# Kernel tuning notes

Hardware: AMD Instinct MI355X
Metric: run time of the kernel (lower is better)

Reference implementation:

```python
import jax, jax.numpy as jnp
import numpy as np
from jax import lax

B, L, D = 2, 4096, 2048
H = 16
DK = D // H  # head qk dim == head v dim == 128
CONV = 4
EPS = 1e-5


def _causal_depthwise_conv(x, w):
    # x: [b, l, c], w: [c, K]; torch-style cross-correlation with left padding K-1
    K = w.shape[1]
    xp = jnp.pad(x, ((0, 0), (K - 1, 0), (0, 0)))
    Lx = x.shape[1]
    y = jnp.zeros_like(x)
    for i in range(K):
        y = y + xp[:, i:i + Lx, :] * w[:, i]
    return y


def _l2norm(x):
    return x / jnp.sqrt(jnp.sum(x * x, axis=-1, keepdims=True) + 1e-12)


def _delta_rule(q, k, v, beta):
    # q,k: [b,h,l,dk]; v: [b,h,l,dv]; beta: [b,h,l]
    b, h, l, dk = q.shape
    dv = v.shape[-1]
    qs = jnp.moveaxis(q, 2, 0)
    ks = jnp.moveaxis(k, 2, 0)
    vs = jnp.moveaxis(v, 2, 0)
    bs = jnp.moveaxis(beta, 2, 0)

    def step(S, inp):
        qt, kt, vt, bt = inp  # [b,h,dk],[b,h,dk],[b,h,dv],[b,h]
        kS = jnp.einsum('bhk,bhkv->bhv', kt, S)
        u = bt[..., None] * (vt - kS)
        S = S + kt[..., None] * u[:, :, None, :]
        o = jnp.einsum('bhk,bhkv->bhv', qt, S)
        return S, o

    S0 = jnp.zeros((b, h, dk, dv), dtype=q.dtype)
    _, os = lax.scan(step, S0, (qs, ks, vs, bs))
    return jnp.moveaxis(os, 0, 2)  # [b,h,l,dv]


def setup_inputs() -> dict:
    key = jax.random.key(0)
    ks = jax.random.split(key, 8)
    s = 0.02
    return {
        'hidden_states': jax.random.normal(ks[0], (B, L, D), jnp.float32),
        'w_cattn': jax.random.normal(ks[1], (D, 3 * D), jnp.float32) * s,
        'wq_conv': jax.random.normal(ks[2], (D, CONV), jnp.float32) * 0.3,
        'wk_conv': jax.random.normal(ks[3], (D, CONV), jnp.float32) * 0.3,
        'wv_conv': jax.random.normal(ks[4], (D, CONV), jnp.float32) * 0.3,
        'w_beta': jax.random.normal(ks[5], (D, H), jnp.float32) * s,
        'o_norm_w': jnp.ones((DK,), jnp.float32),
        'w_o': jax.random.normal(ks[6], (D, D), jnp.float32) * s,
    }


def reference(hidden_states, w_cattn, wq_conv, wk_conv, wv_conv, w_beta, o_norm_w, w_o):
    qkv = hidden_states @ w_cattn  # [b,l,3D]
    q, k, v = jnp.split(qkv, 3, axis=-1)
    # short conv + SiLU activation (qk_activation='silu', v conv always SiLU)
    q = jax.nn.silu(_causal_depthwise_conv(q, wq_conv))
    k = jax.nn.silu(_causal_depthwise_conv(k, wk_conv))
    v = jax.nn.silu(_causal_depthwise_conv(v, wv_conv))
    # b l (h d) -> b h l d
    def to_heads(x):
        return jnp.transpose(x.reshape(B, L, H, -1), (0, 2, 1, 3))
    q, k, v = to_heads(q), to_heads(k), to_heads(v)
    # qk_norm = 'l2'
    q = _l2norm(q)
    k = _l2norm(k)
    beta = jax.nn.sigmoid(hidden_states @ w_beta)  # [b,l,h]
    beta = jnp.transpose(beta, (0, 2, 1))  # [b,h,l]
    o = _delta_rule(q, k, v, beta)  # [b,h,l,dv]
    o = jnp.transpose(o, (0, 2, 1, 3))  # [b,l,h,dv]
    # RMSNorm over head_v_dim
    o = o * lax.rsqrt(jnp.mean(o * o, axis=-1, keepdims=True) + EPS) * o_norm_w
    o = o.reshape(B, L, D)
    return o @ w_o
```

## Files before the change

### kernel.cpp

```cpp
#include <hip/hip_runtime.h>
#include <stdint.h>

#define B_   2
#define L_   4096
#define D_   2048
#define H_   16
#define DK_  128
#define ND3  6144
#define BL_  8192

typedef __bf16 bf16x8 __attribute__((ext_vector_type(8)));
typedef float  f32x4  __attribute__((ext_vector_type(4)));

__device__ __forceinline__ float bf2f(ushort u){ return __uint_as_float(((unsigned)u)<<16); }
__device__ __forceinline__ ushort f2bf(float f){
  unsigned u = __float_as_uint(f);
  unsigned r = u + 0x7FFFu + ((u>>16)&1u);
  return (ushort)(r>>16);
}
__device__ __forceinline__ f32x4 mfma16(bf16x8 a, bf16x8 b, f32x4 c){
  return __builtin_amdgcn_mfma_f32_16x16x32_bf16(a, b, c, 0, 0, 0);
}

#define BAR_LGKM() do{ __builtin_amdgcn_sched_barrier(0); \
  asm volatile("s_waitcnt lgkmcnt(0)" ::: "memory"); \
  __builtin_amdgcn_s_barrier(); \
  __builtin_amdgcn_sched_barrier(0);}while(0)
#define BAR_VMALL() do{ __builtin_amdgcn_sched_barrier(0); \
  asm volatile("s_waitcnt vmcnt(0) lgkmcnt(0)" ::: "memory"); \
  __builtin_amdgcn_s_barrier(); \
  __builtin_amdgcn_sched_barrier(0);}while(0)

__global__ __launch_bounds__(256) void k_cast(const float* __restrict__ x, ushort* __restrict__ y, int n4){
  int i = blockIdx.x*blockDim.x + threadIdx.x;
  int stride = gridDim.x*blockDim.x;
  for (; i < n4; i += stride){
    float4 v = ((const float4*)x)[i];
    ushort4 o; o.x=f2bf(v.x); o.y=f2bf(v.y); o.z=f2bf(v.z); o.w=f2bf(v.w);
    ((ushort4*)y)[i] = o;
  }
}

__global__ __launch_bounds__(256) void k_transpose_cast(const float* __restrict__ in, ushort* __restrict__ out,
                                                        int R, int C){
  __shared__ float tile[32][33];
  int c0 = blockIdx.x*32, r0 = blockIdx.y*32;
  int tx = threadIdx.x, ty = threadIdx.y;
  #pragma unroll
  for (int i=0;i<32;i+=8) tile[ty+i][tx] = in[(size_t)(r0+ty+i)*C + (c0+tx)];
  __syncthreads();
  #pragma unroll
  for (int i=0;i<32;i+=8) out[(size_t)(c0+ty+i)*R + (r0+tx)] = f2bf(tile[tx][ty+i]);
}

template<int OUT_BF16>
__global__ __launch_bounds__(512, 1) void k_gemmks(const ushort* __restrict__ A, const ushort* __restrict__ Bt,
                                                   void* __restrict__ Cv, int M, int N, int K){
  __shared__ ushort LDSB[65536];
  char* lds = (char*)LDSB;
  const int tid = threadIdx.x, lane = tid & 63, w = tid >> 6;
  const int wm = w >> 2, wn = w & 3;
  int nwg = gridDim.x*gridDim.y;
  int id  = blockIdx.y*gridDim.x + blockIdx.x;
  int sw  = ((nwg & 7) == 0) ? ((id & 7)*(nwg >> 3) + (id >> 3)) : id;
  const int bx = sw % gridDim.x, by = sw / gridDim.x;
  const int m0 = by*256, n0 = bx*256;
  const int NT = K >> 6;
  const int NP = NT*2;
  const size_t rowb = (size_t)K*2;

  f32x4 acc[8][4];
  #pragma unroll
  for (int i=0;i<8;i++)
    #pragma unroll
    for (int j=0;j<4;j++) acc[i][j] = (f32x4){0.f,0.f,0.f,0.f};

  const int c0 = tid, c1 = tid + 512;
  const int r0c = ((c0>>6)<<4) + (c0&15), h0 = (c0>>4)&3;
  const int r1c = ((c1>>6)<<4) + (c1&15), h1 = (c1>>4)&3;
  const char* gA = (const char*)A  + (size_t)m0*rowb;
  const char* gB = (const char*)Bt + (size_t)n0*rowb;

  auto stage = [&](int slot, int tile, int s){
    const char* ga = gA + (size_t)tile*128 + s*64;
    const char* gb = gB + (size_t)tile*128 + s*64;
    char* la = lds + slot*32768;
    char* lb = la + 16384;
    __builtin_amdgcn_global_load_lds((const __attribute__((address_space(1))) void*)(ga + (size_t)r0c*rowb + h0*16),
                                     (__attribute__((address_space(3))) void*)(la + c0*16), 16, 0, 0);
    __builtin_amdgcn_global_load_lds((const __attribute__((address_space(1))) void*)(ga + (size_t)r1c*rowb + h1*16),
                                     (__attribute__((address_space(3))) void*)(la + c1*16), 16, 0, 0);
    __builtin_amdgcn_global_load_lds((const __attribute__((address_space(1))) void*)(gb + (size_t)r0c*rowb + h0*16),
                                     (__attribute__((address_space(3))) void*)(lb + c0*16), 16, 0, 0);
    __builtin_amdgcn_global_load_lds((const __attribute__((address_space(1))) void*)(gb + (size_t)r1c*rowb + h1*16),
                                     (__attribute__((address_space(3))) void*)(lb + c1*16), 16, 0, 0);
  };

  stage(0, 0, 0);
  stage(1, 0, 1);
  stage(2, 1, 0);
  __builtin_amdgcn_sched_barrier(0);
  asm volatile("s_waitcnt vmcnt(8)" ::: "memory");
  __builtin_amdgcn_s_barrier();
  __builtin_amdgcn_sched_barrier(0);

  for (int pb = 0; pb < NP; pb += 4){
    #pragma unroll
    for (int q = 0; q < 4; ++q){
      const int p = pb + q;
      const char* base = lds + q*32768;
      bf16x8 af[8], bfr[4];
      #pragma unroll
      for (int i=0;i<4;i++) af[i]  = *(const bf16x8*)(base + (wm*128 + i*16)*64 + lane*16);
      #pragma unroll
      for (int j=0;j<4;j++) bfr[j] = *(const bf16x8*)(base + 16384 + (wn*64 + j*16)*64 + lane*16);
      __builtin_amdgcn_sched_barrier(0);
      #pragma unroll
      for (int i=4;i<8;i++) af[i]  = *(const bf16x8*)(base + (wm*128 + i*16)*64 + lane*16);
      {
        int ps = p + 3;
        int tile = ps >> 1; if (tile >= NT) tile = NT - 1;
        stage(ps & 3, tile, ps & 1);
      }
      __builtin_amdgcn_sched_barrier(0);
      asm volatile("s_waitcnt lgkmcnt(4)" ::: "memory");
      __builtin_amdgcn_sched_barrier(0);
      __builtin_amdgcn_s_setprio(1);
      #pragma unroll
      for (int i=0;i<4;i++)
        #pragma unroll
        for (int j=0;j<4;j++)
          acc[i][j] = mfma16(af[i], bfr[j], acc[i][j]);
      __builtin_amdgcn_sched_barrier(0);
      asm volatile("s_waitcnt lgkmcnt(0)" ::: "memory");
      __builtin_amdgcn_sched_barrier(0);
      #pragma unroll
      for (int i=4;i<8;i++)
        #pragma unroll
        for (int j=0;j<4;j++)
          acc[i][j] = mfma16(af[i], bfr[j], acc[i][j]);
      __builtin_amdgcn_s_setprio(0);
      __builtin_amdgcn_sched_barrier(0);
      asm volatile("s_waitcnt vmcnt(8)" ::: "memory");
      __builtin_amdgcn_s_barrier();
      __builtin_amdgcn_sched_barrier(0);
    }
  }

  const int rbase = m0 + wm*128 + (lane>>4)*4;
  const int cbase = n0 + wn*64 + (lane&15);
  #pragma unroll
  for (int fi=0;fi<8;fi++)
    #pragma unroll
    for (int fj=0;fj<4;fj++)
      #pragma unroll
      for (int r=0;r<4;r++){
        int row = rbase + fi*16 + r;
        int col = cbase + fj*16;
        float v = acc[fi][fj][r];
        if (OUT_BF16) ((ushort*)Cv)[(size_t)row*N + col] = f2bf(v);
        else          ((float*) Cv)[(size_t)row*N + col] = v;
      }
}

__global__ __launch_bounds__(256) void k_wbt(const float* __restrict__ wb, ushort* __restrict__ wbT){
  int d = blockIdx.x*256 + threadIdx.x;
  #pragma unroll
  for (int h=0;h<16;h++) wbT[(size_t)h*2048 + d] = f2bf(wb[(size_t)d*16 + h]);
}

__global__ __launch_bounds__(64) void k_beta2(const ushort* __restrict__ A16, const ushort* __restrict__ wbT,
                                              float* __restrict__ beta){
  const int rt = blockIdx.x;
  const int lane = threadIdx.x;
  const int lr = lane & 15, lk8 = (lane>>4)*8;
  const int r0 = rt*16;
  f32x4 acc0 = (f32x4){0.f,0.f,0.f,0.f};
  f32x4 acc1 = (f32x4){0.f,0.f,0.f,0.f};
  for (int k0=0; k0<2048; k0+=64){
    bf16x8 a0 = *(const bf16x8*)&A16[(size_t)(r0+lr)*2048 + k0 + lk8];
    bf16x8 b0 = *(const bf16x8*)&wbT[(size_t)lr*2048 + k0 + lk8];
    bf16x8 a1 = *(const bf16x8*)&A16[(size_t)(r0+lr)*2048 + k0 + 32 + lk8];
    bf16x8 b1 = *(const bf16x8*)&wbT[(size_t)lr*2048 + k0 + 32 + lk8];
    acc0 = mfma16(a0, b0, acc0);
    acc1 = mfma16(a1, b1, acc1);
  }
  const int h = lane & 15;
  const int rbase = r0 + (lane>>4)*4;
  #pragma unroll
  for (int r=0;r<4;r++){
    int row = rbase + r;
    int b = row >> 12, l = row & 4095;
    float sg = 1.f/(1.f + __expf(-(acc0[r] + acc1[r])));
    beta[((size_t)(b*H_ + h))*L_ + l] = sg;
  }
}

__global__ __launch_bounds__(256) void k_conv2(const ushort* __restrict__ qkv,
      const float* __restrict__ wq, const float* __restrict__ wk, const float* __restrict__ wv,
      ushort* __restrict__ QH, ushort* __restrict__ KH, ushort* __restrict__ VH){
  const int seg = blockIdx.x, part = blockIdx.y, b = blockIdx.z;
  const int t = threadIdx.x;
  const int ch = t*8;
  const int h = t >> 4, d0 = (t & 15)*8;
  const float* wc = (part==0) ? wq : (part==1) ? wk : wv;
  ushort* outs = ((part==0) ? QH : (part==1) ? KH : VH)
                 + ((size_t)(b*H_ + h)*L_)*DK_ + d0;
  const ushort* inp = qkv + ((size_t)b*L_)*ND3 + part*D_ + ch;

  float wgt[4][8];
  #pragma unroll
  for (int j=0;j<8;j++){
    float4 w4 = *(const float4*)&wc[(ch + j)*4];
    wgt[0][j]=w4.x; wgt[1][j]=w4.y; wgt[2][j]=w4.z; wgt[3][j]=w4.w;
  }

  const int l0 = seg*32;
  float x0[8], x1[8], x2[8];
  {
    float* dsts[3] = {x0, x1, x2};
    #pragma unroll
    for (int i=0;i<3;i++){
      int l = l0 - 3 + i;
      float* d = dsts[i];
      if (l >= 0){
        const ushort* p = inp + (size_t)l*ND3;
        ushort4 a = *(const ushort4*)p, c = *(const ushort4*)(p+4);
        d[0]=bf2f(a.x); d[1]=bf2f(a.y); d[2]=bf2f(a.z); d[3]=bf2f(a.w);
        d[4]=bf2f(c.x); d[5]=bf2f(c.y); d[6]=bf2f(c.z); d[7]=bf2f(c.w);
      } else {
        #pragma unroll
        for (int j=0;j<8;j++) d[j] = 0.f;
      }
    }
  }

  for (int i=0;i<32;i++){
    const int l = l0 + i;
    float cur[8];
    {
      const ushort* p = inp + (size_t)l*ND3;
      ushort4 a = *(const ushort4*)p, c = *(const ushort4*)(p+4);
      cur[0]=bf2f(a.x); cur[1]=bf2f(a.y); cur[2]=bf2f(a.z); cur[3]=bf2f(a.w);
      cur[4]=bf2f(c.x); cur[5]=bf2f(c.y); cur[6]=bf2f(c.z); cur[7]=bf2f(c.w);
    }
    float y[8]; float ss = 0.f;
    #pragma unroll
    for (int j=0;j<8;j++){
      float yy = x0[j]*wgt[0][j] + x1[j]*wgt[1][j] + x2[j]*wgt[2][j] + cur[j]*wgt[3][j];
      yy = yy / (1.f + __expf(-yy));
      y[j] = yy; ss += yy*yy;
    }
    if (part < 2){
      #pragma unroll
      for (int m=1;m<16;m<<=1) ss += __shfl_xor(ss, m, 64);
      float sc = rsqrtf(ss + 1e-12f);
      #pragma unroll
      for (int j=0;j<8;j++) y[j] *= sc;
    }
    ushort4 o0, o1;
    o0.x=f2bf(y[0]); o0.y=f2bf(y[1]); o0.z=f2bf(y[2]); o0.w=f2bf(y[3]);
    o1.x=f2bf(y[4]); o1.y=f2bf(y[5]); o1.z=f2bf(y[6]); o1.w=f2bf(y[7]);
    ushort* op = outs + (size_t)l*DK_;
    *(ushort4*)op = o0; *(ushort4*)(op+4) = o1;
    #pragma unroll
    for (int j=0;j<8;j++){ x0[j]=x1[j]; x1[j]=x2[j]; x2[j]=cur[j]; }
  }
}

__global__ __launch_bounds__(64) void k_prep(const ushort* __restrict__ QH, const ushort* __restrict__ KH,
      const float* __restrict__ BETA, ushort* __restrict__ TB, ushort* __restrict__ MM,
      ushort* __restrict__ KT){
  const int bid = blockIdx.x, bh = bid>>6, c = bid&63;
  const int lane = threadIdx.x;
  __shared__ ushort Ks[64][136];
  __shared__ __align__(16) char QA[17408];
  __shared__ float bs[64];
  ushort (*Qs)[136] = (ushort (*)[136])QA;
  float  (*As)[64]  = (float  (*)[64])QA;

  const ushort* kg = KH + ((size_t)bh*L_ + c*64)*DK_;
  const ushort* qg = QH + ((size_t)bh*L_ + c*64)*DK_;
  {
    const uint4* ks4 = (const uint4*)(kg + (size_t)lane*DK_);
    const uint4* qs4 = (const uint4*)(qg + (size_t)lane*DK_);
    uint4* kd = (uint4*)&Ks[lane][0];
    uint4* qd = (uint4*)&Qs[lane][0];
    #pragma unroll
    for (int i=0;i<16;i++){ kd[i] = ks4[i]; qd[i] = qs4[i]; }
    bs[lane] = BETA[(size_t)bh*L_ + c*64 + lane];
  }
  __syncthreads();
  const int lr = lane&15, lk = lane>>4;

  f32x4 gac[4][4];
  #pragma unroll
  for (int i=0;i<4;i++)
    #pragma unroll
    for (int j=0;j<4;j++) gac[i][j] = (f32x4){0.f,0.f,0.f,0.f};
  #pragma unroll
  for (int kk=0;kk<4;kk++){
    bf16x8 fr[4];
    #pragma unroll
    for (int i=0;i<4;i++) fr[i] = *(const bf16x8*)&Ks[i*16+lr][kk*32 + lk*8];
    #pragma unroll
    for (int mi=0;mi<4;mi++)
      #pragma unroll
      for (int ni=0;ni<4;ni++)
        gac[mi][ni] = mfma16(fr[mi], fr[ni], gac[mi][ni]);
  }
  {
    f32x4 mac[4][4];
    #pragma unroll
    for (int i=0;i<4;i++)
      #pragma unroll
      for (int j=0;j<4;j++) mac[i][j] = (f32x4){0.f,0.f,0.f,0.f};
    #pragma unroll
    for (int kk=0;kk<4;kk++){
      bf16x8 frq[4], frk[4];
      #pragma unroll
      for (int i=0;i<4;i++){
        frq[i] = *(const bf16x8*)&Qs[i*16+lr][kk*32 + lk*8];
        frk[i] = *(const bf16x8*)&Ks[i*16+lr][kk*32 + lk*8];
      }
      #pragma unroll
      for (int mi=0;mi<4;mi++)
        #pragma unroll
        for (int ni=0;ni<4;ni++)
          mac[mi][ni] = mfma16(frq[mi], frk[ni], mac[mi][ni]);
    }
    #pragma unroll
    for (int mi=0;mi<4;mi++)
      #pragma unroll
      for (int ni=0;ni<4;ni++)
        #pragma unroll
        for (int r=0;r<4;r++){
          int t = mi*16 + lk*4 + r, s = ni*16 + lr;
          float v = (s <= t) ? mac[mi][ni][r] : 0.f;
          MM[(size_t)bid*4096 + t*64 + s] = f2bf(v);
        }
  }
  __syncthreads();

  #pragma unroll
  for (int mi=0;mi<4;mi++)
    #pragma unroll
    for (int ni=0;ni<4;ni++)
      #pragma unroll
      for (int r=0;r<4;r++){
        int t = mi*16 + lk*4 + r, s = ni*16 + lr;
        As[t][s] = (s < t) ? (bs[t] * gac[mi][ni][r]) : 0.f;
      }
  __syncthreads();

  float rT[64];
  #pragma unroll
  for (int t=0;t<64;t++){
    float arow = As[t][lane];
    float a = (t==lane) ? 1.f : 0.f;
    #pragma unroll
    for (int s=0;s<t;s++){
      float cc = __int_as_float(__builtin_amdgcn_readlane(__float_as_int(arow), s));
      a -= cc * rT[s];
    }
    rT[t] = a;
  }
  {
    float bc = bs[lane];
    #pragma unroll
    for (int t=0;t<64;t++)
      TB[(size_t)bid*4096 + t*64 + lane] = f2bf(rT[t] * bc);
  }
  for (int d2=0; d2<64; d2++){
    unsigned uu = *(const unsigned*)&Ks[lane][2*d2];
    KT[(size_t)bid*8192 + (size_t)(2*d2)*64 + lane]   = (ushort)(uu & 0xffffu);
    KT[(size_t)bid*8192 + (size_t)(2*d2+1)*64 + lane] = (ushort)(uu >> 16);
  }
}

template<int LRB, int GRB, int NB, int XM>
__device__ __forceinline__ void stage_swz(const ushort* __restrict__ g, ushort* l,
                                          int colOff, int w, int lane){
  for (int idx = w; idx < NB/1024; idx += 4){
    int off = idx*1024 + lane*16;
    int row = off / LRB;
    int inner = off & (LRB-1);
    int src = row*GRB + colOff + (inner ^ ((row&XM)<<4));
    __builtin_amdgcn_global_load_lds(
      (const __attribute__((address_space(1))) void*)((const char*)g + src),
      (__attribute__((address_space(3))) void*)((char*)l + idx*1024), 16, 0, 0);
  }
}

__global__ __launch_bounds__(256) void k_chunkrec(const ushort* __restrict__ QH, const ushort* __restrict__ KH,
      const ushort* __restrict__ VH, const ushort* __restrict__ TB, const ushort* __restrict__ MM,
      const ushort* __restrict__ KT, ushort* __restrict__ OH){
  const int p = blockIdx.x;
  const int xg = p & 7, slot = p >> 3;
  const int bh = xg + (slot >> 2)*8;
  const int vq = slot & 3;
  const int tid = threadIdx.x, lane = tid&63, w = tid>>6;
  const int lr = lane&15, lk = lane>>4;
  const int tw = w*16;
  const int dw = w*32;

  __shared__ ushort SM[77824];
  ushort* Stl = SM + 69632;
  ushort* Ztl = SM + 73728;
  ushort* Utl = SM + 75776;

  const ushort* kbase  = KH + ((size_t)bh*L_)*DK_;
  const ushort* qbase  = QH + ((size_t)bh*L_)*DK_;
  const ushort* vbase  = VH + ((size_t)bh*L_)*DK_;
  const ushort* tbase  = TB + ((size_t)bh*64)*4096;
  const ushort* mbase  = MM + ((size_t)bh*64)*4096;
  const ushort* ktbase = KT + ((size_t)bh*64)*8192;
  ushort* obase = OH + ((size_t)bh*L_)*DK_ + vq*32;

  auto stageall = [&](ushort* buf, int c){
    stage_swz<256,256,16384,7>(kbase  + (size_t)c*8192, buf,         0,     w, lane);
    stage_swz<256,256,16384,7>(qbase  + (size_t)c*8192, buf + 8192,  0,     w, lane);
    stage_swz<128,128,16384,7>(ktbase + (size_t)c*8192, buf + 16384, 0,     w, lane);
    stage_swz<128,128, 8192,7>(tbase  + (size_t)c*4096, buf + 24576, 0,     w, lane);
    stage_swz<128,128, 8192,7>(mbase  + (size_t)c*4096, buf + 28672, 0,     w, lane);
    stage_swz< 64,256, 4096,3>(vbase  + (size_t)c*8192, buf + 32768, vq*64, w, lane);
  };

  f32x4 Stf[2][2];
  #pragma unroll
  for (int a=0;a<2;a++)
    #pragma unroll
    for (int b=0;b<2;b++) Stf[a][b] = (f32x4){0.f,0.f,0.f,0.f};

  stageall(SM, 0);
  BAR_VMALL();

  for (int c=0; c<64; ++c){
    ushort* buf  = SM + (c&1)*34816;
    ushort* nbuf = SM + ((c+1)&1)*34816;
    const ushort* Kc  = buf;
    const ushort* Qc  = buf + 8192;
    const ushort* Ktc = buf + 16384;
    const ushort* Tbc = buf + 24576;
    const ushort* Mc  = buf + 28672;
    const ushort* Vc  = buf + 32768;

    if (c+1 < 64) stageall(nbuf, c+1);

    #pragma unroll
    for (int mj=0;mj<2;mj++)
      #pragma unroll
      for (int nd=0;nd<2;nd++)
        #pragma unroll
        for (int r=0;r<4;r++){
          int j = mj*16 + lk*4 + r;
          int d = dw + nd*16 + lr;
          Stl[j*128 + (d ^ ((j&7)<<3))] = f2bf(Stf[mj][nd][r]);
        }
    BAR_LGKM();

    f32x4 xac[2];
    xac[0] = (f32x4){0.f,0.f,0.f,0.f}; xac[1] = (f32x4){0.f,0.f,0.f,0.f};
    #pragma unroll
    for (int kk=0;kk<4;kk++){
      int e = kk*32 + lk*8;
      int ta = tw + lr;
      bf16x8 ak = *(const bf16x8*)&Kc[ta*128 + (e ^ ((ta&7)<<3))];
      #pragma unroll
      for (int ni=0;ni<2;ni++){
        int j = ni*16 + lr;
        bf16x8 bst = *(const bf16x8*)&Stl[j*128 + (e ^ ((j&7)<<3))];
        xac[ni] = mfma16(ak, bst, xac[ni]);
      }
    }
    #pragma unroll
    for (int ni=0;ni<2;ni++)
      #pragma unroll
      for (int r=0;r<4;r++){
        int t = tw + lk*4 + r;
        int j = ni*16 + lr;
        float v = bf2f(Vc[t*32 + (j ^ ((t&3)<<3))]);
        Ztl[j*64 + (t ^ ((j&7)<<3))] = f2bf(v - xac[ni][r]);
      }
    BAR_LGKM();

    f32x4 uac[2];
    uac[0] = (f32x4){0.f,0.f,0.f,0.f}; uac[1] = (f32x4){0.f,0.f,0.f,0.f};
    #pragma unroll
    for (int kk=0;kk<2;kk++){
      int e = kk*32 + lk*8;
      int ta = tw + lr;
      bf16x8 at = *(const bf16x8*)&Tbc[ta*64 + (e ^ ((ta&7)<<3))];
      #pragma unroll
      for (int ni=0;ni<2;ni++){
        int j = ni*16 + lr;
        bf16x8 bz = *(const bf16x8*)&Ztl[j*64 + (e ^ ((j&7)<<3))];
        uac[ni] = mfma16(at, bz, uac[ni]);
      }
    }
    #pragma unroll
    for (int ni=0;ni<2;ni++)
      #pragma unroll
      for (int r=0;r<4;r++){
        int t = tw + lk*4 + r;
        int j = ni*16 + lr;
        Utl[j*64 + (t ^ ((j&7)<<3))] = f2bf(uac[ni][r]);
      }
    BAR_LGKM();

    f32x4 oac[2];
    oac[0] = (f32x4){0.f,0.f,0.f,0.f}; oac[1] = (f32x4){0.f,0.f,0.f,0.f};
    #pragma unroll
    for (int kk=0;kk<4;kk++){
      int e = kk*32 + lk*8;
      int ta = tw + lr;
      bf16x8 aq = *(const bf16x8*)&Qc[ta*128 + (e ^ ((ta&7)<<3))];
      #pragma unroll
      for (int ni=0;ni<2;ni++){
        int j = ni*16 + lr;
        bf16x8 bst = *(const bf16x8*)&Stl[j*128 + (e ^ ((j&7)<<3))];
        oac[ni] = mfma16(aq, bst, oac[ni]);
      }
    }
    #pragma unroll
    for (int kk=0;kk<2;kk++){
      int e = kk*32 + lk*8;
      int ta = tw + lr;
      bf16x8 am = *(const bf16x8*)&Mc[ta*64 + (e ^ ((ta&7)<<3))];
      #pragma unroll
      for (int ni=0;ni<2;ni++){
        int j = ni*16 + lr;
        bf16x8 bu = *(const bf16x8*)&Utl[j*64 + (e ^ ((j&7)<<3))];
        oac[ni] = mfma16(am, bu, oac[ni]);
      }
    }
    #pragma unroll
    for (int ni=0;ni<2;ni++)
      #pragma unroll
      for (int r=0;r<4;r++){
        int t = tw + lk*4 + r;
        int j = ni*16 + lr;
        obase[(size_t)(c*64 + t)*DK_ + j] = f2bf(oac[ni][r]);
      }

    #pragma unroll
    for (int kk=0;kk<2;kk++){
      int e = kk*32 + lk*8;
      bf16x8 au[2], bk[2];
      #pragma unroll
      for (int mj=0;mj<2;mj++){ int j = mj*16 + lr; au[mj] = *(const bf16x8*)&Utl[j*64 + (e ^ ((j&7)<<3))]; }
      #pragma unroll
      for (int nd=0;nd<2;nd++){ int d = dw + nd*16 + lr; bk[nd] = *(const bf16x8*)&Ktc[d*64 + (e ^ ((d&7)<<3))]; }
      #pragma unroll
      for (int mj=0;mj<2;mj++)
        #pragma unroll
        for (int nd=0;nd<2;nd++)
          Stf[mj][nd] = mfma16(au[mj], bk[nd], Stf[mj][nd]);
    }
    BAR_VMALL();
  }
}

__global__ __launch_bounds__(256) void k_norm(const ushort* __restrict__ OH, const float* __restrict__ gw,
                                              ushort* __restrict__ O2){
  const int blk = blockIdx.x;
  const int b = blk >> 12, l = blk & 4095;
  const int t = threadIdx.x;
  const int h = t >> 4, d0 = (t & 15) * 8;
  const ushort* ip = OH + ((size_t)(b*H_ + h)*L_ + l)*DK_ + d0;
  ushort4 a = *(const ushort4*)ip, c = *(const ushort4*)(ip+4);
  float x[8];
  x[0]=bf2f(a.x); x[1]=bf2f(a.y); x[2]=bf2f(a.z); x[3]=bf2f(a.w);
  x[4]=bf2f(c.x); x[5]=bf2f(c.y); x[6]=bf2f(c.z); x[7]=bf2f(c.w);
  float ss = 0.f;
  #pragma unroll
  for (int j=0;j<8;j++) ss += x[j]*x[j];
  #pragma unroll
  for (int m=1;m<16;m<<=1) ss += __shfl_xor(ss, m, 64);
  float sc = rsqrtf(ss * (1.f/128.f) + 1e-5f);
  ushort* opp = O2 + (size_t)blk*D_ + h*DK_ + d0;
  ushort4 o0, o1;
  o0.x=f2bf(x[0]*sc*gw[d0+0]); o0.y=f2bf(x[1]*sc*gw[d0+1]);
  o0.z=f2bf(x[2]*sc*gw[d0+2]); o0.w=f2bf(x[3]*sc*gw[d0+3]);
  o1.x=f2bf(x[4]*sc*gw[d0+4]); o1.y=f2bf(x[5]*sc*gw[d0+5]);
  o1.z=f2bf(x[6]*sc*gw[d0+6]); o1.w=f2bf(x[7]*sc*gw[d0+7]);
  *(ushort4*)opp = o0; *(ushort4*)(opp+4) = o1;
}

extern "C" void kernel_launch(void* const* d_in, const int* in_sizes, int n_in,
                              void* d_out, int out_size, void* d_ws, size_t ws_size,
                              hipStream_t stream) {
  (void)in_sizes; (void)n_in; (void)out_size; (void)ws_size;
  const float* hidden  = (const float*)d_in[0];
  const float* w_cattn = (const float*)d_in[1];
  const float* wq_conv = (const float*)d_in[2];
  const float* wk_conv = (const float*)d_in[3];
  const float* wv_conv = (const float*)d_in[4];
  const float* w_beta  = (const float*)d_in[5];
  const float* o_nw    = (const float*)d_in[6];
  const float* w_o     = (const float*)d_in[7];
  float* out = (float*)d_out;

  char* W = (char*)d_ws;
  ushort* A16   = (ushort*)(W);
  ushort* WcatT = (ushort*)(W + 33554432u);
  ushort* WoT   = (ushort*)(W + 33554432u);
  float*  BETA  = (float*) (W + 41943040u);
  ushort* WBT   = (ushort*)(W + 42467328u);
  ushort* QKV   = (ushort*)(W + 58720256u);
  ushort* TB    = (ushort*)(W + 58720256u);
  ushort* MM    = (ushort*)(W + 75497472u);
  ushort* KT    = (ushort*)(W + 92274688u);
  ushort* O2    = (ushort*)(W + 125829120u);
  ushort* QH    = (ushort*)(W + 159383552u);
  ushort* KH    = (ushort*)(W + 192937984u);
  ushort* VH    = (ushort*)(W + 226492416u);
  ushort* OH = A16;

  k_cast<<<4096, 256, 0, stream>>>(hidden, A16, (BL_*D_)/4);
  k_transpose_cast<<<dim3(ND3/32, D_/32), dim3(32,8), 0, stream>>>(w_cattn, WcatT, D_, ND3);
  k_gemmks<1><<<dim3(ND3/256, BL_/256), 512, 0, stream>>>(A16, WcatT, QKV, BL_, ND3, D_);
  k_transpose_cast<<<dim3(D_/32, D_/32), dim3(32,8), 0, stream>>>(w_o, WoT, D_, D_);
  k_wbt<<<8, 256, 0, stream>>>(w_beta, WBT);
  k_beta2<<<512, 64, 0, stream>>>(A16, WBT, BETA);
  k_conv2<<<dim3(128, 3, 2), 256, 0, stream>>>(QKV, wq_conv, wk_conv, wv_conv, QH, KH, VH);
  k_prep<<<2048, 64, 0, stream>>>(QH, KH, BETA, TB, MM, KT);
  k_chunkrec<<<128, 256, 0, stream>>>(QH, KH, VH, TB, MM, KT, OH);
  k_norm<<<BL_, 256, 0, stream>>>(OH, o_nw, O2);
  k_gemmks<0><<<dim3(D_/256, BL_/256), 512, 0, stream>>>(O2, WoT, out, BL_, D_, D_);
}
```

Baseline: 614.3 us.

## Split chunk recurrence across 8 value slices per head to double block count

The chunked delta-rule recurrence kernel now splits each head's value dimension into 8 slices of 16 columns instead of 4 slices of 32. This doubles the grid from 128 to 256 blocks so more compute units on the GPU are busy, and it halves per-block MFMA work and shared memory. In exchange, each block still loads the full K, Q, K-transpose, T and M chunk tiles, so redundant global-to-LDS traffic for those shared operands doubles.

```diff
diff --git a/kernel.cpp b/kernel.cpp
--- a/kernel.cpp
+++ b/kernel.cpp
@@ -396,18 +396,18 @@
       const ushort* __restrict__ VH, const ushort* __restrict__ TB, const ushort* __restrict__ MM,
       const ushort* __restrict__ KT, ushort* __restrict__ OH){
   const int p = blockIdx.x;
-  const int xg = p & 7, slot = p >> 3;
-  const int bh = xg + (slot >> 2)*8;
-  const int vq = slot & 3;
+  const int xg = p & 7, s = p >> 3;
+  const int bh = xg + (s >> 3)*8;
+  const int vo = s & 7;
   const int tid = threadIdx.x, lane = tid&63, w = tid>>6;
   const int lr = lane&15, lk = lane>>4;
   const int tw = w*16;
   const int dw = w*32;
 
-  __shared__ ushort SM[77824];
-  ushort* Stl = SM + 69632;
-  ushort* Ztl = SM + 73728;
-  ushort* Utl = SM + 75776;
+  __shared__ ushort SM[71680];
+  ushort* Stl = SM + 67584;
+  ushort* Ztl = SM + 69632;
+  ushort* Utl = SM + 70656;
 
   const ushort* kbase  = KH + ((size_t)bh*L_)*DK_;
   const ushort* qbase  = QH + ((size_t)bh*L_)*DK_;
@@ -415,7 +415,7 @@
   const ushort* tbase  = TB + ((size_t)bh*64)*4096;
   const ushort* mbase  = MM + ((size_t)bh*64)*4096;
   const ushort* ktbase = KT + ((size_t)bh*64)*8192;
-  ushort* obase = OH + ((size_t)bh*L_)*DK_ + vq*32;
+  ushort* obase = OH + ((size_t)bh*L_)*DK_ + vo*16;
 
   auto stageall = [&](ushort* buf, int c){
     stage_swz<256,256,16384,7>(kbase  + (size_t)c*8192, buf,         0,     w, lane);
@@ -423,21 +423,19 @@
     stage_swz<128,128,16384,7>(ktbase + (size_t)c*8192, buf + 16384, 0,     w, lane);
     stage_swz<128,128, 8192,7>(tbase  + (size_t)c*4096, buf + 24576, 0,     w, lane);
     stage_swz<128,128, 8192,7>(mbase  + (size_t)c*4096, buf + 28672, 0,     w, lane);
-    stage_swz< 64,256, 4096,3>(vbase  + (size_t)c*8192, buf + 32768, vq*64, w, lane);
+    stage_swz< 32,256, 2048,0>(vbase  + (size_t)c*8192, buf + 32768, vo*32, w, lane);
   };
 
-  f32x4 Stf[2][2];
-  #pragma unroll
-  for (int a=0;a<2;a++)
-    #pragma unroll
-    for (int b=0;b<2;b++) Stf[a][b] = (f32x4){0.f,0.f,0.f,0.f};
+  f32x4 Stf[2];
+  Stf[0] = (f32x4){0.f,0.f,0.f,0.f};
+  Stf[1] = (f32x4){0.f,0.f,0.f,0.f};
 
   stageall(SM, 0);
   BAR_VMALL();
 
   for (int c=0; c<64; ++c){
-    ushort* buf  = SM + (c&1)*34816;
-    ushort* nbuf = SM + ((c+1)&1)*34816;
+    ushort* buf  = SM + (c&1)*33792;
+    ushort* nbuf = SM + ((c+1)&1)*33792;
     const ushort* Kc  = buf;
     const ushort* Qc  = buf + 8192;
     const ushort* Ktc = buf + 16384;
@@ -448,114 +446,84 @@
     if (c+1 < 64) stageall(nbuf, c+1);
 
     #pragma unroll
-    for (int mj=0;mj<2;mj++)
-      #pragma unroll
-      for (int nd=0;nd<2;nd++)
-        #pragma unroll
-        for (int r=0;r<4;r++){
-          int j = mj*16 + lk*4 + r;
-          int d = dw + nd*16 + lr;
-          Stl[j*128 + (d ^ ((j&7)<<3))] = f2bf(Stf[mj][nd][r]);
-        }
+    for (int nd=0;nd<2;nd++)
+      #pragma unroll
+      for (int r=0;r<4;r++){
+        int j = lk*4 + r;
+        int d = dw + nd*16 + lr;
+        Stl[j*128 + (d ^ ((j&7)<<3))] = f2bf(Stf[nd][r]);
+      }
     BAR_LGKM();
 
-    f32x4 xac[2];
-    xac[0] = (f32x4){0.f,0.f,0.f,0.f}; xac[1] = (f32x4){0.f,0.f,0.f,0.f};
+    f32x4 xac = (f32x4){0.f,0.f,0.f,0.f};
     #pragma unroll
     for (int kk=0;kk<4;kk++){
       int e = kk*32 + lk*8;
       int ta = tw + lr;
-      bf16x8 ak = *(const bf16x8*)&Kc[ta*128 + (e ^ ((ta&7)<<3))];
-      #pragma unroll
-      for (int ni=0;ni<2;ni++){
-        int j = ni*16 + lr;
-        bf16x8 bst = *(const bf16x8*)&Stl[j*128 + (e ^ ((j&7)<<3))];
-        xac[ni] = mfma16(ak, bst, xac[ni]);
-      }
-    }
-    #pragma unroll
-    for (int ni=0;ni<2;ni++)
-      #pragma unroll
-      for (int r=0;r<4;r++){
-        int t = tw + lk*4 + r;
-        int j = ni*16 + lr;
-        float v = bf2f(Vc[t*32 + (j ^ ((t&3)<<3))]);
-        Ztl[j*64 + (t ^ ((j&7)<<3))] = f2bf(v - xac[ni][r]);
-      }
+      bf16x8 ak  = *(const bf16x8*)&Kc[ta*128 + (e ^ ((ta&7)<<3))];
+      bf16x8 bst = *(const bf16x8*)&Stl[lr*128 + (e ^ ((lr&7)<<3))];
+      xac = mfma16(ak, bst, xac);
+    }
+    #pragma unroll
+    for (int r=0;r<4;r++){
+      int t = tw + lk*4 + r;
+      int j = lr;
+      float v = bf2f(Vc[t*16 + j]);
+      Ztl[j*64 + (t ^ ((j&7)<<3))] = f2bf(v - xac[r]);
+    }
     BAR_LGKM();
 
-    f32x4 uac[2];
-    uac[0] = (f32x4){0.f,0.f,0.f,0.f}; uac[1] = (f32x4){0.f,0.f,0.f,0.f};
+    f32x4 uac = (f32x4){0.f,0.f,0.f,0.f};
     #pragma unroll
     for (int kk=0;kk<2;kk++){
       int e = kk*32 + lk*8;
       int ta = tw + lr;
       bf16x8 at = *(const bf16x8*)&Tbc[ta*64 + (e ^ ((ta&7)<<3))];
-      #pragma unroll
-      for (int ni=0;ni<2;ni++){
-        int j = ni*16 + lr;
-        bf16x8 bz = *(const bf16x8*)&Ztl[j*64 + (e ^ ((j&7)<<3))];
-        uac[ni] = mfma16(at, bz, uac[ni]);
-      }
-    }
-    #pragma unroll
-    for (int ni=0;ni<2;ni++)
-      #pragma unroll
-      for (int r=0;r<4;r++){
-        int t = tw + lk*4 + r;
-        int j = ni*16 + lr;
-        Utl[j*64 + (t ^ ((j&7)<<3))] = f2bf(uac[ni][r]);
-      }
+      bf16x8 bz = *(const bf16x8*)&Ztl[lr*64 + (e ^ ((lr&7)<<3))];
+      uac = mfma16(at, bz, uac);
+    }
+    #pragma unroll
+    for (int r=0;r<4;r++){
+      int t = tw + lk*4 + r;
+      int j = lr;
+      Utl[j*64 + (t ^ ((j&7)<<3))] = f2bf(uac[r]);
+    }
     BAR_LGKM();
 
-    f32x4 oac[2];
-    oac[0] = (f32x4){0.f,0.f,0.f,0.f}; oac[1] = (f32x4){0.f,0.f,0.f,0.f};
+    f32x4 oac = (f32x4){0.f,0.f,0.f,0.f};
     #pragma unroll
     for (int kk=0;kk<4;kk++){
       int e = kk*32 + lk*8;
       int ta = tw + lr;
-      bf16x8 aq = *(const bf16x8*)&Qc[ta*128 + (e ^ ((ta&7)<<3))];
-      #pragma unroll
-      for (int ni=0;ni<2;ni++){
-        int j = ni*16 + lr;
-        bf16x8 bst = *(const bf16x8*)&Stl[j*128 + (e ^ ((j&7)<<3))];
-        oac[ni] = mfma16(aq, bst, oac[ni]);
-      }
+      bf16x8 aq  = *(const bf16x8*)&Qc[ta*128 + (e ^ ((ta&7)<<3))];
+      bf16x8 bst = *(const bf16x8*)&Stl[lr*128 + (e ^ ((lr&7)<<3))];
+      oac = mfma16(aq, bst, oac);
     }
     #pragma unroll
     for (int kk=0;kk<2;kk++){
       int e = kk*32 + lk*8;
       int ta = tw + lr;
       bf16x8 am = *(const bf16x8*)&Mc[ta*64 + (e ^ ((ta&7)<<3))];
-      #pragma unroll
-      for (int ni=0;ni<2;ni++){
-        int j = ni*16 + lr;
-        bf16x8 bu = *(const bf16x8*)&Utl[j*64 + (e ^ ((j&7)<<3))];
-        oac[ni] = mfma16(am, bu, oac[ni]);
-      }
-    }
-    #pragma unroll
-    for (int ni=0;ni<2;ni++)
-      #pragma unroll
-      for (int r=0;r<4;r++){
-        int t = tw + lk*4 + r;
-        int j = ni*16 + lr;
-        obase[(size_t)(c*64 + t)*DK_ + j] = f2bf(oac[ni][r]);
-      }
+      bf16x8 bu = *(const bf16x8*)&Utl[lr*64 + (e ^ ((lr&7)<<3))];
+      oac = mfma16(am, bu, oac);
+    }
+    #pragma unroll
+    for (int r=0;r<4;r++){
+      int t = tw + lk*4 + r;
+      int j = lr;
+      obase[(size_t)(c*64 + t)*DK_ + j] = f2bf(oac[r]);
+    }
 
     #pragma unroll
     for (int kk=0;kk<2;kk++){
       int e = kk*32 + lk*8;
-      bf16x8 au[2], bk[2];
-      #pragma unroll
-      for (int mj=0;mj<2;mj++){ int j = mj*16 + lr; au[mj] = *(const bf16x8*)&Utl[j*64 + (e ^ ((j&7)<<3))]; }
-      #pragma unroll
-      for (int nd=0;nd<2;nd++){ int d = dw + nd*16 + lr; bk[nd] = *(const bf16x8*)&Ktc[d*64 + (e ^ ((d&7)<<3))]; }
-      #pragma unroll
-      for (int mj=0;mj<2;mj++)
-        #pragma unroll
-        for (int nd=0;nd<2;nd++)
-          Stf[mj][nd] = mfma16(au[mj], bk[nd], Stf[mj][nd]);
+      bf16x8 au = *(const bf16x8*)&Utl[lr*64 + (e ^ ((lr&7)<<3))];
+      #pragma unroll
+      for (int nd=0;nd<2;nd++){
+        int d = dw + nd*16 + lr;
+        bf16x8 bk = *(const bf16x8*)&Ktc[d*64 + (e ^ ((d&7)<<3))];
+        Stf[nd] = mfma16(au, bk, Stf[nd]);
+      }
     }
     BAR_VMALL();
   }
@@ -625,7 +593,7 @@
   k_beta2<<<512, 64, 0, stream>>>(A16, WBT, BETA);
   k_conv2<<<dim3(128, 3, 2), 256, 0, stream>>>(QKV, wq_conv, wk_conv, wv_conv, QH, KH, VH);
   k_prep<<<2048, 64, 0, stream>>>(QH, KH, BETA, TB, MM, KT);
-  k_chunkrec<<<128, 256, 0, stream>>>(QH, KH, VH, TB, MM, KT, OH);
+  k_chunkrec<<<256, 256, 0, stream>>>(QH, KH, VH, TB, MM, KT, OH);
   k_norm<<<BL_, 256, 0, stream>>>(OH, o_nw, O2);
   k_gemmks<0><<<dim3(D_/256, BL_/256), 512, 0, stream>>>(O2, WoT, out, BL_, D_, D_);
 }
```

Result: faster. 580.0 us (-5.6%).
